# Optimization experiments

Measured on AMD Instinct MI355X. Metric: run time of the kernel, lower is better.

## Reference

```python
import jax, jax.numpy as jnp
import numpy as np

HIDDEN = 1024

def setup_inputs() -> dict:
    key = jax.random.key(0)
    ks = jax.random.split(key, 7)
    scale = 1.0 / np.sqrt(HIDDEN)
    x = jax.random.normal(ks[0], (4, 2048, HIDDEN), dtype=jnp.float32)
    Wq = jax.random.uniform(ks[1], (HIDDEN, HIDDEN), jnp.float32, -scale, scale)
    bq = jax.random.uniform(ks[2], (HIDDEN,), jnp.float32, -scale, scale)
    Wk = jax.random.uniform(ks[3], (HIDDEN, HIDDEN), jnp.float32, -scale, scale)
    bk = jax.random.uniform(ks[4], (HIDDEN,), jnp.float32, -scale, scale)
    Wv = jax.random.uniform(ks[5], (HIDDEN, HIDDEN), jnp.float32, -scale, scale)
    bv = jax.random.uniform(ks[6], (HIDDEN,), jnp.float32, -scale, scale)
    return {"x": x, "Wq": Wq, "bq": bq, "Wk": Wk, "bk": bk, "Wv": Wv, "bv": bv}

def reference(x, Wq, bq, Wk, bk, Wv, bv):
    # x: [n, t, e]; weights stored as [in, out] so y = x @ W + b
    q = jnp.einsum('nte,ef->ntf', x, Wq) + bq
    k = jnp.einsum('nte,ef->ntf', x, Wk) + bk
    v = jnp.einsum('nte,ef->ntf', x, Wv) + bv
    scores = jnp.einsum('nqe,nke->nqk', q, k)  # unscaled, as in the original
    alpha = jax.nn.softmax(scores, axis=2)
    return jnp.einsum('nqk,nke->nqe', alpha, v)
```

## Files before the change

kernel.cpp:

```cpp
#include <hip/hip_runtime.h>
#include <stdint.h>

typedef __attribute__((ext_vector_type(4))) float f32x4;
typedef __attribute__((ext_vector_type(8))) _Float16 f16x8;

#define HIDDEN 1024
#define SEQ 2048
#define NB 4

__device__ inline unsigned short f2h_bits(float f) {
    _Float16 h = (_Float16)f;
    return __builtin_bit_cast(unsigned short, h);
}

__device__ inline void gload16(const void* g, void* l) {
    __builtin_amdgcn_global_load_lds(
        (const __attribute__((address_space(1))) unsigned int*)g,
        (__attribute__((address_space(3))) unsigned int*)l,
        16, 0, 0);
}

template<int N> __device__ inline void waitvm() {
    if constexpr (N == 0) asm volatile("s_waitcnt vmcnt(0)" ::: "memory");
    else if constexpr (N == 3) asm volatile("s_waitcnt vmcnt(3)" ::: "memory");
    else if constexpr (N == 4) asm volatile("s_waitcnt vmcnt(4)" ::: "memory");
    else if constexpr (N == 6) asm volatile("s_waitcnt vmcnt(6)" ::: "memory");
    else if constexpr (N == 8) asm volatile("s_waitcnt vmcnt(8)" ::: "memory");
    else static_assert(N == 0, "bad vmcnt");
}
__device__ inline void waitlgkm0() { asm volatile("s_waitcnt lgkmcnt(0)" ::: "memory"); }

template<int BM, int BN, int WM, int WN, int BIAS_MODE, bool OUT_F16, int MINW>
__global__ __launch_bounds__(WM * WN * 64, MINW) void gemm8p(
    const unsigned short* __restrict__ A, int lda,
    const unsigned short* __restrict__ Bt, int ldb,
    const float* __restrict__ bias,
    void* __restrict__ Cptr, int ldc, int K,
    long long aBatch, long long bBatch, long long cBatch)
{
    constexpr int THREADS = WM * WN * 64;
    constexpr int MR = BM / (WM * 16);
    constexpr int NRW = BN / (WN * 16);
    constexpr int MH = MR / 2;
    constexpr int LA = 4 * BM / THREADS;
    constexpr int LB = 4 * BN / THREADS;
    constexpr int LP = LA + LB;
    constexpr int ASLICE = BM * 32;
    constexpr int BSLICE = BN * 32;
    constexpr int BOFF = 4 * ASLICE;

    extern __shared__ unsigned short lds[];

    const int tid = threadIdx.x, lane = tid & 63, wave = tid >> 6;
    const int wr = wave / WN, wc = wave % WN;
    const int fr = lane & 15, fq = lane >> 4;

    const int gx = gridDim.x, gy = gridDim.y;
    const int nwg = gx * gy * gridDim.z;
    const int id = (blockIdx.z * gy + blockIdx.y) * gx + blockIdx.x;
    const int id2 = (id & 7) * (nwg >> 3) + (id >> 3);
    const int bx = id2 % gx;
    const int by = (id2 / gx) % gy;
    const long long bz = id2 / (gx * gy);

    const unsigned short* Ab = A + bz * aBatch + (long long)(by * BM) * lda;
    const unsigned short* Bb = Bt + bz * bBatch + (long long)(bx * BN) * ldb;

    const unsigned short* sA[LA]; int dA[LA];
    #pragma unroll
    for (int i = 0; i < LA; ++i) {
        int c = i * THREADS + tid; int r = c >> 2; int ls = (c & 3) ^ ((r >> 1) & 3);
        sA[i] = Ab + (long long)r * lda + ls * 8;
        dA[i] = (i * THREADS + wave * 64) * 16;
    }
    const unsigned short* sB[LB]; int dB[LB];
    #pragma unroll
    for (int i = 0; i < LB; ++i) {
        int c = i * THREADS + tid; int r = c >> 2; int ls = (c & 3) ^ ((r >> 1) & 3);
        sB[i] = Bb + (long long)r * ldb + ls * 8;
        dB[i] = (i * THREADS + wave * 64) * 16;
    }

    auto stage = [&](int q) {
        int slot = q & 3;
        int kof = q * 32;
        #pragma unroll
        for (int i = 0; i < LA; ++i)
            gload16(sA[i] + kof, (char*)lds + slot * (ASLICE * 2) + dA[i]);
        #pragma unroll
        for (int i = 0; i < LB; ++i)
            gload16(sB[i] + kof, (char*)lds + (BOFF + slot * BSLICE) * 2 + dB[i]);
    };

    const int NPAIR = K / 32;
    stage(0); stage(1); stage(2);

    f32x4 acc[MR][NRW] = {};

    for (int p = 0; p < NPAIR; ++p) {
        if (p == NPAIR - 1) waitvm<0>();
        else if (p == NPAIR - 2) waitvm<LP>();
        else waitvm<2 * LP>();
        __builtin_amdgcn_s_barrier();
        __builtin_amdgcn_sched_barrier(0);

        const int slot = p & 3;
        const unsigned short* as = lds + slot * ASLICE;
        const unsigned short* bs = lds + BOFF + slot * BSLICE;

        f16x8 af[MR], bf[NRW];
        #pragma unroll
        for (int n = 0; n < NRW; ++n) {
            int r = wc * (BN / WN) + n * 16 + fr;
            int es = fq ^ ((r >> 1) & 3);
            bf[n] = *(const f16x8*)&bs[r * 32 + es * 8];
        }
        #pragma unroll
        for (int m = 0; m < MH; ++m) {
            int r = wr * (BM / WM) + m * 16 + fr;
            int es = fq ^ ((r >> 1) & 3);
            af[m] = *(const f16x8*)&as[r * 32 + es * 8];
        }
        if (p + 3 < NPAIR) stage(p + 3);
        waitlgkm0();
        __builtin_amdgcn_sched_barrier(0);
        __builtin_amdgcn_s_setprio(1);
        #pragma unroll
        for (int m = 0; m < MH; ++m)
            #pragma unroll
            for (int n = 0; n < NRW; ++n)
                acc[m][n] = __builtin_amdgcn_mfma_f32_16x16x32_f16(af[m], bf[n], acc[m][n], 0, 0, 0);
        __builtin_amdgcn_s_setprio(0);

        #pragma unroll
        for (int m = MH; m < MR; ++m) {
            int r = wr * (BM / WM) + m * 16 + fr;
            int es = fq ^ ((r >> 1) & 3);
            af[m] = *(const f16x8*)&as[r * 32 + es * 8];
        }
        __builtin_amdgcn_s_barrier();
        waitlgkm0();
        __builtin_amdgcn_sched_barrier(0);
        __builtin_amdgcn_s_setprio(1);
        #pragma unroll
        for (int m = MH; m < MR; ++m)
            #pragma unroll
            for (int n = 0; n < NRW; ++n)
                acc[m][n] = __builtin_amdgcn_mfma_f32_16x16x32_f16(af[m], bf[n], acc[m][n], 0, 0, 0);
        __builtin_amdgcn_s_setprio(0);
    }

    const int row0 = by * BM + wr * (BM / WM);
    const int col0 = bx * BN + wc * (BN / WN);
    #pragma unroll
    for (int m = 0; m < MR; ++m)
        #pragma unroll
        for (int n = 0; n < NRW; ++n)
            #pragma unroll
            for (int i = 0; i < 4; ++i) {
                int r = row0 + m * 16 + fq * 4 + i;
                int c = col0 + n * 16 + fr;
                float v = acc[m][n][i];
                if constexpr (BIAS_MODE == 1) v += bias[c];
                if constexpr (BIAS_MODE == 2) v += bias[r];
                if constexpr (OUT_F16)
                    ((unsigned short*)Cptr + bz * cBatch)[(long long)r * ldc + c] = f2h_bits(v);
                else
                    ((float*)Cptr + bz * cBatch)[(long long)r * ldc + c] = v;
            }
}

__global__ __launch_bounds__(256) void cvt_f32_f16(const float* __restrict__ in,
                                                   unsigned short* __restrict__ out, int n8)
{
    int i = blockIdx.x * blockDim.x + threadIdx.x;
    if (i >= n8) return;
    const float4* p = (const float4*)in + (long long)i * 2;
    float4 a = p[0], b = p[1];
    ushort4 o0, o1;
    o0.x = f2h_bits(a.x); o0.y = f2h_bits(a.y); o0.z = f2h_bits(a.z); o0.w = f2h_bits(a.w);
    o1.x = f2h_bits(b.x); o1.y = f2h_bits(b.y); o1.z = f2h_bits(b.z); o1.w = f2h_bits(b.w);
    ushort4* o = (ushort4*)out + (long long)i * 2;
    o[0] = o0; o[1] = o1;
}

__global__ void transpose_cvt(const float* __restrict__ in, unsigned short* __restrict__ out,
                              int R, int C)
{
    __shared__ unsigned short t[32][33];
    const int bx = blockIdx.x * 32;
    const int by = blockIdx.y * 32;
    const int xT = threadIdx.x, yT = threadIdx.y;
    #pragma unroll
    for (int i = 0; i < 32; i += 8)
        t[yT + i][xT] = f2h_bits(in[(long long)(by + yT + i) * C + bx + xT]);
    __syncthreads();
    #pragma unroll
    for (int i = 0; i < 32; i += 8)
        out[(long long)(bx + yT + i) * R + by + xT] = t[xT][yT + i];
}

__global__ void concat_bias2(const float* __restrict__ bq, const float* __restrict__ bk,
                             float* __restrict__ cb)
{
    int i = threadIdx.x;
    cb[i] = bq[i];
    cb[HIDDEN + i] = bk[i];
}

__global__ __launch_bounds__(256) void softmax_inplace(float* __restrict__ S)
{
    const int tid = threadIdx.x;
    float* row = S + (long long)blockIdx.x * SEQ;
    float4 a = ((const float4*)row)[tid];
    float4 b = ((const float4*)row)[tid + 256];
    float vv[8] = {a.x, a.y, a.z, a.w, b.x, b.y, b.z, b.w};

    float mx = vv[0];
    #pragma unroll
    for (int j = 1; j < 8; ++j) mx = fmaxf(mx, vv[j]);
    #pragma unroll
    for (int o = 32; o > 0; o >>= 1) mx = fmaxf(mx, __shfl_xor(mx, o));
    __shared__ float redm[4], reds[4];
    if ((tid & 63) == 0) redm[tid >> 6] = mx;
    __syncthreads();
    mx = fmaxf(fmaxf(redm[0], redm[1]), fmaxf(redm[2], redm[3]));

    float ev[8], sum = 0.f;
    #pragma unroll
    for (int j = 0; j < 8; ++j) { ev[j] = __expf(vv[j] - mx); sum += ev[j]; }
    #pragma unroll
    for (int o = 32; o > 0; o >>= 1) sum += __shfl_xor(sum, o);
    if ((tid & 63) == 0) reds[tid >> 6] = sum;
    __syncthreads();
    sum = reds[0] + reds[1] + reds[2] + reds[3];
    float inv = 1.0f / sum;

    unsigned short* rb = (unsigned short*)row;
    ushort4 o0, o1;
    o0.x = f2h_bits(ev[0] * inv); o0.y = f2h_bits(ev[1] * inv);
    o0.z = f2h_bits(ev[2] * inv); o0.w = f2h_bits(ev[3] * inv);
    o1.x = f2h_bits(ev[4] * inv); o1.y = f2h_bits(ev[5] * inv);
    o1.z = f2h_bits(ev[6] * inv); o1.w = f2h_bits(ev[7] * inv);
    *(ushort4*)&rb[(long long)tid * 4] = o0;
    *(ushort4*)&rb[((long long)tid + 256) * 4] = o1;
}

extern "C" void kernel_launch(void* const* d_in, const int* in_sizes, int n_in,
                              void* d_out, int out_size, void* d_ws, size_t ws_size,
                              hipStream_t stream)
{
    (void)in_sizes; (void)n_in; (void)out_size; (void)ws_size;
    const float* x  = (const float*)d_in[0];
    const float* Wq = (const float*)d_in[1];
    const float* bq = (const float*)d_in[2];
    const float* Wk = (const float*)d_in[3];
    const float* bk = (const float*)d_in[4];
    const float* Wv = (const float*)d_in[5];
    const float* bv = (const float*)d_in[6];
    float* out = (float*)d_out;

    (void)hipFuncSetAttribute(reinterpret_cast<const void*>(&gemm8p<256, 256, 2, 4, 1, true, 2>),
                              hipFuncAttributeMaxDynamicSharedMemorySize, 131072);
    (void)hipFuncSetAttribute(reinterpret_cast<const void*>(&gemm8p<128, 256, 2, 4, 2, true, 2>),
                              hipFuncAttributeMaxDynamicSharedMemorySize, 98304);
    (void)hipFuncSetAttribute(reinterpret_cast<const void*>(&gemm8p<128, 256, 2, 4, 0, false, 2>),
                              hipFuncAttributeMaxDynamicSharedMemorySize, 98304);
    (void)hipFuncSetAttribute(reinterpret_cast<const void*>(&gemm8p<128, 128, 2, 2, 0, false, 2>),
                              hipFuncAttributeMaxDynamicSharedMemorySize, 65536);

    char* ws = (char*)d_ws;
    const long long MTOT = (long long)NB * SEQ;

    unsigned short* qk = (unsigned short*)ws;
    unsigned short* vt = (unsigned short*)(ws + (size_t)MTOT * 2048 * 2);
    char* sreg = ws + (size_t)MTOT * 2048 * 2 + (size_t)HIDDEN * MTOT * 2;
    unsigned short* wt = (unsigned short*)sreg;
    float* cb = (float*)(sreg + (size_t)3 * HIDDEN * HIDDEN * 2);
    unsigned short* xh = (unsigned short*)(sreg + (size_t)3 * HIDDEN * HIDDEN * 2 + 8192);
    float* S = (float*)sreg;

    {
        int n8 = (int)(MTOT * HIDDEN / 8);
        cvt_f32_f16<<<dim3((n8 + 255) / 256), 256, 0, stream>>>(x, xh, n8);
    }
    dim3 tb(32, 8), tg(HIDDEN / 32, HIDDEN / 32);
    transpose_cvt<<<tg, tb, 0, stream>>>(Wq, wt,                       HIDDEN, HIDDEN);
    transpose_cvt<<<tg, tb, 0, stream>>>(Wk, wt +     HIDDEN * HIDDEN, HIDDEN, HIDDEN);
    transpose_cvt<<<tg, tb, 0, stream>>>(Wv, wt + 2 * HIDDEN * HIDDEN, HIDDEN, HIDDEN);
    concat_bias2<<<1, 1024, 0, stream>>>(bq, bk, cb);

    gemm8p<256, 256, 2, 4, 1, true, 2><<<dim3(2048 / 256, (unsigned)(MTOT / 256), 1), 512, 131072, stream>>>(
        xh, HIDDEN, wt, HIDDEN, cb, qk, 2048, HIDDEN, 0, 0, 0);

    gemm8p<128, 256, 2, 4, 2, true, 2><<<dim3((unsigned)(MTOT / 256), HIDDEN / 128, 1), 512, 98304, stream>>>(
        wt + 2 * HIDDEN * HIDDEN, HIDDEN, xh, HIDDEN, bv, vt, (int)MTOT, HIDDEN, 0, 0, 0);

    for (int b0 = 0; b0 < NB; b0 += 2) {
        const unsigned short* q  = qk + (long long)b0 * SEQ * 2048;
        const unsigned short* km = q + HIDDEN;
        gemm8p<128, 256, 2, 4, 0, false, 2><<<dim3(SEQ / 256, SEQ / 128, 2), 512, 98304, stream>>>(
            q, 2048, km, 2048, nullptr, S, SEQ, HIDDEN,
            (long long)SEQ * 2048, (long long)SEQ * 2048, (long long)SEQ * SEQ);
        softmax_inplace<<<dim3(2 * SEQ), 256, 0, stream>>>(S);
        const unsigned short* P = (const unsigned short*)S;
        const unsigned short* Bv = vt + (long long)b0 * SEQ;
        float* Ob = out + (long long)b0 * SEQ * HIDDEN;
        gemm8p<128, 128, 2, 2, 0, false, 2><<<dim3(HIDDEN / 128, SEQ / 128, 2), 256, 65536, stream>>>(
            P, 2 * SEQ, Bv, (int)MTOT, nullptr, Ob, HIDDEN, SEQ,
            (long long)SEQ * 2 * SEQ, (long long)SEQ, (long long)SEQ * HIDDEN);
    }
}
```

Before: 202.0 us.

## Store scores in fp16, batch all heads per launch, and reorder LDS fragment loads

The score GEMM now writes fp16 instead of fp32, so the softmax reads and writes half-width rows and works in place on compact fp16 storage. The per-pair loop is replaced by single launches over all four batches with larger 256x256 and 256x128 tiles. Inside the GEMM main loop, the second half of the A fragments is fetched before the first MFMA group, guarded by a partial lgkmcnt wait, and the mid-iteration barrier is removed. This aims to cut memory traffic and launch count and to hide LDS latency. It risks fp16 overflow on unscaled scores and a possible LDS race from the dropped barrier.

```diff
diff --git a/kernel.cpp b/kernel.cpp
--- a/kernel.cpp
+++ b/kernel.cpp
@@ -3,6 +3,7 @@
 
 typedef __attribute__((ext_vector_type(4))) float f32x4;
 typedef __attribute__((ext_vector_type(8))) _Float16 f16x8;
+typedef __attribute__((ext_vector_type(8))) unsigned short u16x8;
 
 #define HIDDEN 1024
 #define SEQ 2048
@@ -11,6 +12,9 @@
 __device__ inline unsigned short f2h_bits(float f) {
     _Float16 h = (_Float16)f;
     return __builtin_bit_cast(unsigned short, h);
+}
+__device__ inline float h2f(unsigned short u) {
+    return (float)__builtin_bit_cast(_Float16, u);
 }
 
 __device__ inline void gload16(const void* g, void* l) {
@@ -28,7 +32,12 @@
     else if constexpr (N == 8) asm volatile("s_waitcnt vmcnt(8)" ::: "memory");
     else static_assert(N == 0, "bad vmcnt");
 }
-__device__ inline void waitlgkm0() { asm volatile("s_waitcnt lgkmcnt(0)" ::: "memory"); }
+template<int N> __device__ inline void waitlgkm() {
+    if constexpr (N == 0) asm volatile("s_waitcnt lgkmcnt(0)" ::: "memory");
+    else if constexpr (N == 2) asm volatile("s_waitcnt lgkmcnt(2)" ::: "memory");
+    else if constexpr (N == 4) asm volatile("s_waitcnt lgkmcnt(4)" ::: "memory");
+    else static_assert(N == 0, "bad lgkmcnt");
+}
 
 template<int BM, int BN, int WM, int WN, int BIAS_MODE, bool OUT_F16, int MINW>
 __global__ __launch_bounds__(WM * WN * 64, MINW) void gemm8p(
@@ -122,7 +131,14 @@
             af[m] = *(const f16x8*)&as[r * 32 + es * 8];
         }
         if (p + 3 < NPAIR) stage(p + 3);
-        waitlgkm0();
+        #pragma unroll
+        for (int m = MH; m < MR; ++m) {
+            int r = wr * (BM / WM) + m * 16 + fr;
+            int es = fq ^ ((r >> 1) & 3);
+            af[m] = *(const f16x8*)&as[r * 32 + es * 8];
+        }
+
+        waitlgkm<MR - MH>();
         __builtin_amdgcn_sched_barrier(0);
         __builtin_amdgcn_s_setprio(1);
         #pragma unroll
@@ -131,15 +147,8 @@
             for (int n = 0; n < NRW; ++n)
                 acc[m][n] = __builtin_amdgcn_mfma_f32_16x16x32_f16(af[m], bf[n], acc[m][n], 0, 0, 0);
         __builtin_amdgcn_s_setprio(0);
-
-        #pragma unroll
-        for (int m = MH; m < MR; ++m) {
-            int r = wr * (BM / WM) + m * 16 + fr;
-            int es = fq ^ ((r >> 1) & 3);
-            af[m] = *(const f16x8*)&as[r * 32 + es * 8];
-        }
-        __builtin_amdgcn_s_barrier();
-        waitlgkm0();
+        __builtin_amdgcn_sched_barrier(0);
+        waitlgkm<0>();
         __builtin_amdgcn_sched_barrier(0);
         __builtin_amdgcn_s_setprio(1);
         #pragma unroll
@@ -208,13 +217,14 @@
     cb[HIDDEN + i] = bk[i];
 }
 
-__global__ __launch_bounds__(256) void softmax_inplace(float* __restrict__ S)
+__global__ __launch_bounds__(256) void softmax_h(unsigned short* __restrict__ S)
 {
     const int tid = threadIdx.x;
-    float* row = S + (long long)blockIdx.x * SEQ;
-    float4 a = ((const float4*)row)[tid];
-    float4 b = ((const float4*)row)[tid + 256];
-    float vv[8] = {a.x, a.y, a.z, a.w, b.x, b.y, b.z, b.w};
+    unsigned short* row = S + (long long)blockIdx.x * SEQ;
+    u16x8 hv = *(const u16x8*)&row[tid * 8];
+    float vv[8];
+    #pragma unroll
+    for (int j = 0; j < 8; ++j) vv[j] = h2f(hv[j]);
 
     float mx = vv[0];
     #pragma unroll
@@ -236,14 +246,10 @@
     sum = reds[0] + reds[1] + reds[2] + reds[3];
     float inv = 1.0f / sum;
 
-    unsigned short* rb = (unsigned short*)row;
-    ushort4 o0, o1;
-    o0.x = f2h_bits(ev[0] * inv); o0.y = f2h_bits(ev[1] * inv);
-    o0.z = f2h_bits(ev[2] * inv); o0.w = f2h_bits(ev[3] * inv);
-    o1.x = f2h_bits(ev[4] * inv); o1.y = f2h_bits(ev[5] * inv);
-    o1.z = f2h_bits(ev[6] * inv); o1.w = f2h_bits(ev[7] * inv);
-    *(ushort4*)&rb[(long long)tid * 4] = o0;
-    *(ushort4*)&rb[((long long)tid + 256) * 4] = o1;
+    u16x8 ov;
+    #pragma unroll
+    for (int j = 0; j < 8; ++j) ov[j] = f2h_bits(ev[j] * inv);
+    *(u16x8*)&row[tid * 8] = ov;
 }
 
 extern "C" void kernel_launch(void* const* d_in, const int* in_sizes, int n_in,
@@ -262,12 +268,12 @@
 
     (void)hipFuncSetAttribute(reinterpret_cast<const void*>(&gemm8p<256, 256, 2, 4, 1, true, 2>),
                               hipFuncAttributeMaxDynamicSharedMemorySize, 131072);
+    (void)hipFuncSetAttribute(reinterpret_cast<const void*>(&gemm8p<256, 256, 2, 4, 0, true, 2>),
+                              hipFuncAttributeMaxDynamicSharedMemorySize, 131072);
     (void)hipFuncSetAttribute(reinterpret_cast<const void*>(&gemm8p<128, 256, 2, 4, 2, true, 2>),
                               hipFuncAttributeMaxDynamicSharedMemorySize, 98304);
-    (void)hipFuncSetAttribute(reinterpret_cast<const void*>(&gemm8p<128, 256, 2, 4, 0, false, 2>),
+    (void)hipFuncSetAttribute(reinterpret_cast<const void*>(&gemm8p<256, 128, 2, 4, 0, false, 2>),
                               hipFuncAttributeMaxDynamicSharedMemorySize, 98304);
-    (void)hipFuncSetAttribute(reinterpret_cast<const void*>(&gemm8p<128, 128, 2, 2, 0, false, 2>),
-                              hipFuncAttributeMaxDynamicSharedMemorySize, 65536);
 
     char* ws = (char*)d_ws;
     const long long MTOT = (long long)NB * SEQ;
@@ -278,7 +284,7 @@
     unsigned short* wt = (unsigned short*)sreg;
     float* cb = (float*)(sreg + (size_t)3 * HIDDEN * HIDDEN * 2);
     unsigned short* xh = (unsigned short*)(sreg + (size_t)3 * HIDDEN * HIDDEN * 2 + 8192);
-    float* S = (float*)sreg;
+    unsigned short* S = (unsigned short*)sreg;
 
     {
         int n8 = (int)(MTOT * HIDDEN / 8);
@@ -296,18 +302,13 @@
     gemm8p<128, 256, 2, 4, 2, true, 2><<<dim3((unsigned)(MTOT / 256), HIDDEN / 128, 1), 512, 98304, stream>>>(
         wt + 2 * HIDDEN * HIDDEN, HIDDEN, xh, HIDDEN, bv, vt, (int)MTOT, HIDDEN, 0, 0, 0);
 
-    for (int b0 = 0; b0 < NB; b0 += 2) {
-        const unsigned short* q  = qk + (long long)b0 * SEQ * 2048;
-        const unsigned short* km = q + HIDDEN;
-        gemm8p<128, 256, 2, 4, 0, false, 2><<<dim3(SEQ / 256, SEQ / 128, 2), 512, 98304, stream>>>(
-            q, 2048, km, 2048, nullptr, S, SEQ, HIDDEN,
-            (long long)SEQ * 2048, (long long)SEQ * 2048, (long long)SEQ * SEQ);
-        softmax_inplace<<<dim3(2 * SEQ), 256, 0, stream>>>(S);
-        const unsigned short* P = (const unsigned short*)S;
-        const unsigned short* Bv = vt + (long long)b0 * SEQ;
-        float* Ob = out + (long long)b0 * SEQ * HIDDEN;
-        gemm8p<128, 128, 2, 2, 0, false, 2><<<dim3(HIDDEN / 128, SEQ / 128, 2), 256, 65536, stream>>>(
-            P, 2 * SEQ, Bv, (int)MTOT, nullptr, Ob, HIDDEN, SEQ,
-            (long long)SEQ * 2 * SEQ, (long long)SEQ, (long long)SEQ * HIDDEN);
-    }
-}
+    gemm8p<256, 256, 2, 4, 0, true, 2><<<dim3(SEQ / 256, SEQ / 256, NB), 512, 131072, stream>>>(
+        qk, 2048, qk + HIDDEN, 2048, nullptr, S, SEQ, HIDDEN,
+        (long long)SEQ * 2048, (long long)SEQ * 2048, (long long)SEQ * SEQ);
+
+    softmax_h<<<dim3(NB * SEQ), 256, 0, stream>>>(S);
+
+    gemm8p<256, 128, 2, 4, 0, false, 2><<<dim3(HIDDEN / 128, SEQ / 256, NB), 512, 98304, stream>>>(
+        S, SEQ, vt, (int)MTOT, nullptr, out, HIDDEN, SEQ,
+        (long long)SEQ * SEQ, (long long)SEQ, (long long)SEQ * HIDDEN);
+}
```

Result: faster. 173.2 us (-14.3%).
